# Optimization experiments

Hardware: AMD Instinct MI355X
Metric: run time of the kernel (lower is better)

## Reference

```python
import jax, jax.numpy as jnp
import numpy as np

DIM = 768
N_HEADS = 12
HEAD_DIM = DIM // N_HEADS  # 64
SEQ = 4096
ROPE_THETA = 10000.0  # local layer (layer_id=1)
WINDOW = 128          # local_attention; mask is distance <= WINDOW // 2


def setup_inputs() -> dict:
    key = jax.random.key(0)
    k1, k2, k3 = jax.random.split(key, 3)
    x = jax.random.normal(k1, (1, SEQ, DIM), dtype=jnp.float32)
    position_ids = jnp.arange(SEQ, dtype=jnp.int64 if jax.config.jax_enable_x64 else jnp.int32).reshape(1, SEQ)
    wqkv = jax.random.normal(k2, (3 * DIM, DIM), dtype=jnp.float32) * 0.02
    wo = jax.random.normal(k3, (DIM, DIM), dtype=jnp.float32) * 0.02
    return {"x": x, "position_ids": position_ids, "wqkv": wqkv, "wo": wo}


def _rope_cos_sin(position_ids):
    # inv_freq over even dims, freqs duplicated to full head_dim
    inv_freq = 1.0 / (ROPE_THETA ** (jnp.arange(0, HEAD_DIM, 2, dtype=jnp.float32) / HEAD_DIM))
    pos = position_ids.reshape(-1).astype(jnp.float32)           # [S]
    freqs = pos[:, None] * inv_freq[None, :]                      # [S, hd/2]
    freqs = jnp.concatenate([freqs, freqs], axis=-1)              # [S, hd]
    return jnp.cos(freqs)[None, None], jnp.sin(freqs)[None, None]  # [1,1,S,hd]


def _rotate_half(t):
    h = t.shape[-1] // 2
    return jnp.concatenate([-t[..., h:], t[..., :h]], axis=-1)


def reference(x, position_ids, wqkv, wo):
    bsz, seq_len, _ = x.shape
    qkv = jnp.einsum("bsd,ed->bse", x, wqkv)                      # [B,S,3*dim]
    qkv = qkv.reshape(bsz, seq_len, 3, N_HEADS, HEAD_DIM)
    qkv = jnp.transpose(qkv, (0, 3, 2, 1, 4))                      # [B,H,3,S,hd]
    q, k, v = qkv[:, :, 0], qkv[:, :, 1], qkv[:, :, 2]             # [B,H,S,hd]

    cos, sin = _rope_cos_sin(position_ids)
    q = q * cos + _rotate_half(q) * sin
    k = k * cos + _rotate_half(k) * sin

    scale = HEAD_DIM ** -0.5
    scores = jnp.einsum("bhqd,bhkd->bhqk", q, k) * scale           # [B,H,S,S]

    # sliding-window mask: |i - j| <= WINDOW // 2
    idx = jnp.arange(seq_len)
    dist = jnp.abs(idx[None, :] - idx[:, None])                    # [S,S]
    window_mask = dist <= (WINDOW // 2)
    scores = jnp.where(window_mask[None, None], scores, -jnp.inf)

    attn = jax.nn.softmax(scores, axis=-1)
    out = jnp.einsum("bhqk,bhkd->bhqd", attn, v)                   # [B,H,S,hd]
    out = jnp.transpose(out, (0, 2, 1, 3)).reshape(bsz, seq_len, DIM)
    out = jnp.einsum("bsd,ed->bse", out, wo)
    return out
```

## Files before the change

kernel.cpp:

```cpp
#include <hip/hip_runtime.h>
#include <math.h>

#define SEQ 4096
#define DIM 768
#define NH 12
#define HD 64
#define QKV_N 2304
#define HALF_WIN 64

typedef __attribute__((ext_vector_type(8))) short bf16x8;
typedef __attribute__((ext_vector_type(4))) float floatx4;

__device__ __forceinline__ unsigned short f2bf(float f) {
    unsigned u = __float_as_uint(f);
    unsigned r = (u + 0x7fffu + ((u >> 16) & 1u)) >> 16;
    return (unsigned short)r;
}

__device__ __forceinline__ void gld16(const void* g, void* l) {
    __builtin_amdgcn_global_load_lds(
        (const __attribute__((address_space(1))) unsigned*)g,
        (__attribute__((address_space(3))) unsigned*)l, 16, 0, 0);
}

__device__ __forceinline__ void fast_sc(float x, float* s, float* c) {
    float r = x * 0.15915494309189535f;
    r = r - floorf(r);
    *s = __builtin_amdgcn_sinf(r);
    *c = __builtin_amdgcn_cosf(r);
}

__global__ __launch_bounds__(256) void cast3_bf16(const float* __restrict__ x,
                                                  const float* __restrict__ wqkv,
                                                  const float* __restrict__ wo,
                                                  unsigned short* __restrict__ dst,
                                                  int nx4, int nw4, int ntot4) {
    int i = blockIdx.x * 256 + threadIdx.x;
    if (i >= ntot4) return;
    const float4* src;
    int off;
    if (i < nx4)            { src = (const float4*)x;    off = i; }
    else if (i < nx4 + nw4) { src = (const float4*)wqkv; off = i - nx4; }
    else                    { src = (const float4*)wo;   off = i - nx4 - nw4; }
    float4 v = src[off];
    ushort4 r;
    r.x = f2bf(v.x); r.y = f2bf(v.y); r.z = f2bf(v.z); r.w = f2bf(v.w);
    *(ushort4*)(dst + (size_t)i * 4) = r;
}

__global__ __launch_bounds__(256) void gemm_qkv_rope(const unsigned short* __restrict__ A,
                                                     const unsigned short* __restrict__ B,
                                                     unsigned short* __restrict__ qr,
                                                     unsigned short* __restrict__ kr,
                                                     unsigned short* __restrict__ vt) {
    __shared__ __align__(16) short smem[8192];
    short* As = smem;
    short* Bs = smem + 4096;
    const int t  = threadIdx.x;
    const int wv = t >> 6, ln = t & 63;
    const int bm0 = blockIdx.y * 64;
    const int bn0 = blockIdx.x * 64;
    const int lrow = ln >> 3;
    const int lu   = ln & 7;
    const int frow = ln & 15;
    const int q    = ln >> 4;
    const int K = DIM;

    const unsigned short* gptr[4];
    short* lptr[4];
#pragma unroll
    for (int i = 0; i < 4; i++) {
        int idx = wv * 4 + i;
        int c   = (idx < 8) ? idx : idx - 8;
        int row = c * 8 + lrow;
        int g   = (lu ^ (row & 7)) << 3;
        if (idx < 8) {
            gptr[i] = A + (size_t)(bm0 + row) * K + g;
            lptr[i] = As + c * 512;
        } else {
            gptr[i] = B + (size_t)(bn0 + row) * K + g;
            lptr[i] = Bs + c * 512;
        }
    }

    floatx4 acc[4];
#pragma unroll
    for (int j = 0; j < 4; j++) acc[j] = (floatx4){0.f, 0.f, 0.f, 0.f};

    for (int k0 = 0; k0 < K; k0 += 64) {
        __syncthreads();
#pragma unroll
        for (int i = 0; i < 4; i++) gld16(gptr[i] + k0, (void*)lptr[i]);
        __syncthreads();

#pragma unroll
        for (int ks = 0; ks < 2; ks++) {
            bf16x8 af, bfr[4];
            {
                int ra = wv * 16 + frow;
                af = *(const bf16x8*)&As[ra * 64 + (((ks * 4 + q) ^ (ra & 7)) << 3)];
            }
#pragma unroll
            for (int nt = 0; nt < 4; nt++) {
                int rb = nt * 16 + frow;
                bfr[nt] = *(const bf16x8*)&Bs[rb * 64 + (((ks * 4 + q) ^ (rb & 7)) << 3)];
            }
#pragma unroll
            for (int nt = 0; nt < 4; nt++)
                acc[nt] = __builtin_amdgcn_mfma_f32_16x16x32_bf16(
                    af, bfr[nt], acc[nt], 0, 0, 0);
        }
    }

    const int cn = frow;
    const int part = (bn0 >= 1536) ? 2 : (bn0 >= 768 ? 1 : 0);

    if (part < 2) {
        const int colw = bn0 - part * 768;
        const int h = colw >> 6;
        unsigned short* dst = (part == 0 ? qr : kr) + (size_t)h * SEQ * HD;
        const float invf0 = exp2f(-(float)cn * 0.4152410118609203f);
        const float invf1 = exp2f(-(float)(cn + 16) * 0.4152410118609203f);
        const int sbase = bm0 + wv * 16 + q * 4;
#pragma unroll
        for (int r = 0; r < 4; r++) {
            float ss = (float)(sbase + r);
            float sn0, cs0, sn1, cs1;
            fast_sc(ss * invf0, &sn0, &cs0);
            fast_sc(ss * invf1, &sn1, &cs1);
            float o0 = acc[0][r] * cs0 - acc[2][r] * sn0;
            float o1 = acc[1][r] * cs1 - acc[3][r] * sn1;
            float o2 = acc[2][r] * cs0 + acc[0][r] * sn0;
            float o3 = acc[3][r] * cs1 + acc[1][r] * sn1;
            unsigned short* p = dst + (size_t)(sbase + r) * HD + cn;
            p[0]  = f2bf(o0);
            p[16] = f2bf(o1);
            p[32] = f2bf(o2);
            p[48] = f2bf(o3);
        }
    } else {
        short* vstage = smem;
        __syncthreads();
#pragma unroll
        for (int nt = 0; nt < 4; nt++) {
            int d    = nt * 16 + cn;
            int sloc = wv * 16 + q * 4;
            ushort4 pk;
            pk.x = f2bf(acc[nt][0]);
            pk.y = f2bf(acc[nt][1]);
            pk.z = f2bf(acc[nt][2]);
            pk.w = f2bf(acc[nt][3]);
            *(ushort4*)&vstage[d * 72 + sloc] = pk;
        }
        __syncthreads();
        const int dr = t >> 2, sh = (t & 3) * 16;
        const int vcol = bn0 - 1536 + dr;
        unsigned short* vp = vt + (size_t)vcol * SEQ + bm0 + sh;
        *(uint4*)(vp)     = *(const uint4*)&vstage[dr * 72 + sh];
        *(uint4*)(vp + 8) = *(const uint4*)&vstage[dr * 72 + sh + 8];
    }
}

__global__ __launch_bounds__(256) void gemm_out(const unsigned short* __restrict__ A,
                                                const unsigned short* __restrict__ B,
                                                float* __restrict__ C,
                                                int M, int N, int K) {
    __shared__ __align__(16) short As[64 * 64];
    __shared__ __align__(16) short Bs[64 * 64];
    const int t  = threadIdx.x;
    const int wv = t >> 6, ln = t & 63;
    const int wm = wv >> 1, wn = wv & 1;
    const int bm0 = blockIdx.y * 64;
    const int bn0 = blockIdx.x * 64;
    const int lrow = ln >> 3;
    const int lu   = ln & 7;
    const int frow = ln & 15;
    const int q    = ln >> 4;

    const unsigned short* gptr[4];
    short* lptr[4];
#pragma unroll
    for (int i = 0; i < 4; i++) {
        int idx = wv * 4 + i;
        int c   = (idx < 8) ? idx : idx - 8;
        int row = c * 8 + lrow;
        int g   = (lu ^ (row & 7)) << 3;
        if (idx < 8) {
            gptr[i] = A + (size_t)(bm0 + row) * K + g;
            lptr[i] = As + c * 512;
        } else {
            gptr[i] = B + (size_t)(bn0 + row) * K + g;
            lptr[i] = Bs + c * 512;
        }
    }

    floatx4 acc[2][2];
#pragma unroll
    for (int i = 0; i < 2; i++)
#pragma unroll
        for (int j = 0; j < 2; j++) acc[i][j] = (floatx4){0.f, 0.f, 0.f, 0.f};

    for (int k0 = 0; k0 < K; k0 += 64) {
        __syncthreads();
#pragma unroll
        for (int i = 0; i < 4; i++) gld16(gptr[i] + k0, (void*)lptr[i]);
        __syncthreads();

#pragma unroll
        for (int ks = 0; ks < 2; ks++) {
            bf16x8 af[2], bfr[2];
#pragma unroll
            for (int mt = 0; mt < 2; mt++) {
                int ra = wm * 32 + mt * 16 + frow;
                af[mt] = *(const bf16x8*)&As[ra * 64 + (((ks * 4 + q) ^ (ra & 7)) << 3)];
            }
#pragma unroll
            for (int nt = 0; nt < 2; nt++) {
                int rb = wn * 32 + nt * 16 + frow;
                bfr[nt] = *(const bf16x8*)&Bs[rb * 64 + (((ks * 4 + q) ^ (rb & 7)) << 3)];
            }
#pragma unroll
            for (int mt = 0; mt < 2; mt++)
#pragma unroll
                for (int nt = 0; nt < 2; nt++)
                    acc[mt][nt] = __builtin_amdgcn_mfma_f32_16x16x32_bf16(
                        af[mt], bfr[nt], acc[mt][nt], 0, 0, 0);
        }
    }

    const int cn = ln & 15;
    const int rb4 = (ln >> 4) * 4;
#pragma unroll
    for (int mt = 0; mt < 2; mt++) {
#pragma unroll
        for (int nt = 0; nt < 2; nt++) {
            floatx4 v = acc[mt][nt];
            float* cp = C + (size_t)(bm0 + wm * 32 + mt * 16 + rb4) * N +
                        bn0 + wn * 32 + nt * 16 + cn;
#pragma unroll
            for (int r = 0; r < 4; r++) cp[(size_t)r * N] = v[r];
        }
    }
}

__global__ __launch_bounds__(512) void attn_mfma(const unsigned short* __restrict__ Q,
                                                 const unsigned short* __restrict__ K,
                                                 const unsigned short* __restrict__ Vt,
                                                 unsigned short* __restrict__ Out) {
    __shared__ __align__(16) short lds[16384];
    short* Ks  = lds;
    short* Vts = lds + 4096;
    short* Pb  = lds + 8192;
    const int t  = threadIdx.x;
    const int wv = t >> 6, ln = t & 63;
    const int h  = blockIdx.x, qs = blockIdx.y * 128;
    const int frow = ln & 15, qd = ln >> 4;
    const int rl = ln >> 3, uu = ln & 7;
    const unsigned short* Qh = Q + (size_t)h * SEQ * HD;
    const unsigned short* Kh = K + (size_t)h * SEQ * HD;
    const unsigned short* Vh = Vt + (size_t)h * HD * SEQ;

    const unsigned short* qp = Qh + (size_t)(qs + wv * 16 + frow) * HD;
    bf16x8 af0 = *(const bf16x8*)(qp + qd * 8);
    bf16x8 af1 = *(const bf16x8*)(qp + (qd + 4) * 8);

    floatx4 accO[4];
#pragma unroll
    for (int i = 0; i < 4; i++) accO[i] = (floatx4){0.f, 0.f, 0.f, 0.f};
    float m_r[4] = {-1e30f, -1e30f, -1e30f, -1e30f};
    float l_r[4] = {0.f, 0.f, 0.f, 0.f};

    const int qlo = wv * 16;

    for (int c = 0; c < 4; c++) {
        const int kb  = qs - 64 + c * 64;
        const int kbc = kb < 0 ? 0 : (kb > SEQ - 64 ? SEQ - 64 : kb);
        __syncthreads();
        {
            int row = wv * 8 + rl;
            int g = uu ^ ((row + (row >> 3)) & 7);
            gld16(Kh + (size_t)(kbc + row) * HD + g * 8, (void*)(Ks + wv * 512));
            gld16(Vh + (size_t)row * SEQ + kbc + g * 8, (void*)(Vts + wv * 512));
        }
        __syncthreads();

        const int klo0 = c * 64 - 64;
        bool live_kt[4];
        bool any_live = false;
#pragma unroll
        for (int kt = 0; kt < 4; kt++) {
            int d0 = qlo - (klo0 + kt * 16);
            live_kt[kt] = (d0 <= 64) && (d0 >= -64);
            any_live = any_live || live_kt[kt];
        }

        float sv[4][4];
        float cm[4] = {-1e30f, -1e30f, -1e30f, -1e30f};
        if (any_live) {
#pragma unroll
            for (int kt = 0; kt < 4; kt++) {
                if (live_kt[kt]) {
                    int brow = kt * 16 + frow;
                    int bz = (brow + (brow >> 3)) & 7;
                    bf16x8 b0 = *(const bf16x8*)&Ks[brow * 64 + ((qd ^ bz) << 3)];
                    bf16x8 b1 = *(const bf16x8*)&Ks[brow * 64 + (((qd + 4) ^ bz) << 3)];
                    floatx4 z = (floatx4){0.f, 0.f, 0.f, 0.f};
                    z = __builtin_amdgcn_mfma_f32_16x16x32_bf16(af0, b0, z, 0, 0, 0);
                    z = __builtin_amdgcn_mfma_f32_16x16x32_bf16(af1, b1, z, 0, 0, 0);
                    int gk = kb + kt * 16 + frow;
#pragma unroll
                    for (int r = 0; r < 4; r++) {
                        int gq = qs + wv * 16 + qd * 4 + r;
                        int dd = gq - gk;
                        bool valid = (gk >= 0) && (gk < SEQ) &&
                                     (dd <= HALF_WIN) && (dd >= -HALF_WIN);
                        float x = valid ? z[r] * 0.125f : -1e30f;
                        sv[kt][r] = x;
                        cm[r] = fmaxf(cm[r], x);
                    }
                } else {
#pragma unroll
                    for (int r = 0; r < 4; r++) sv[kt][r] = -1e30f;
                }
            }
#pragma unroll
            for (int off = 1; off < 16; off <<= 1)
#pragma unroll
                for (int r = 0; r < 4; r++)
                    cm[r] = fmaxf(cm[r], __shfl_xor(cm[r], off, 64));
            float al[4], ls[4];
#pragma unroll
            for (int r = 0; r < 4; r++) {
                float mn = fmaxf(m_r[r], cm[r]);
                al[r] = __expf(m_r[r] - mn);
                m_r[r] = mn;
                ls[r] = 0.f;
            }
            const int qrb = wv * 16 + qd * 4;
#pragma unroll
            for (int kt = 0; kt < 4; kt++) {
                int klocal = kt * 16 + frow;
                int ku = klocal >> 3;
                if (live_kt[kt]) {
#pragma unroll
                    for (int r = 0; r < 4; r++) {
                        float p = (sv[kt][r] > -1e29f) ? __expf(sv[kt][r] - m_r[r]) : 0.f;
                        ls[r] += p;
                        int qrow = qrb + r;
                        int pz = (qrow + (qrow >> 3)) & 7;
                        Pb[qrow * 64 + ((ku ^ pz) << 3) + (klocal & 7)] = (short)f2bf(p);
                    }
                } else {
#pragma unroll
                    for (int r = 0; r < 4; r++) {
                        int qrow = qrb + r;
                        int pz = (qrow + (qrow >> 3)) & 7;
                        Pb[qrow * 64 + ((ku ^ pz) << 3) + (klocal & 7)] = 0;
                    }
                }
            }
#pragma unroll
            for (int off = 1; off < 16; off <<= 1)
#pragma unroll
                for (int r = 0; r < 4; r++) ls[r] += __shfl_xor(ls[r], off, 64);
#pragma unroll
            for (int r = 0; r < 4; r++) l_r[r] = l_r[r] * al[r] + ls[r];
#pragma unroll
            for (int dt = 0; dt < 4; dt++)
#pragma unroll
                for (int r = 0; r < 4; r++) accO[dt][r] *= al[r];
        }
        __syncthreads();

        if (any_live) {
            const int prow = wv * 16 + frow;
            const int pz2 = (prow + (prow >> 3)) & 7;
            bf16x8 pa0 = *(const bf16x8*)&Pb[prow * 64 + ((qd ^ pz2) << 3)];
            bf16x8 pa1 = *(const bf16x8*)&Pb[prow * 64 + (((qd + 4) ^ pz2) << 3)];
#pragma unroll
            for (int dt = 0; dt < 4; dt++) {
                int vrow = dt * 16 + frow;
                int vz = (vrow + (vrow >> 3)) & 7;
                bf16x8 v0 = *(const bf16x8*)&Vts[vrow * 64 + ((qd ^ vz) << 3)];
                bf16x8 v1 = *(const bf16x8*)&Vts[vrow * 64 + (((qd + 4) ^ vz) << 3)];
                accO[dt] = __builtin_amdgcn_mfma_f32_16x16x32_bf16(pa0, v0, accO[dt], 0, 0, 0);
                accO[dt] = __builtin_amdgcn_mfma_f32_16x16x32_bf16(pa1, v1, accO[dt], 0, 0, 0);
            }
        }
    }

    __syncthreads();
    short* Ob = lds;
    float linv[4];
#pragma unroll
    for (int r = 0; r < 4; r++) linv[r] = 1.0f / l_r[r];
#pragma unroll
    for (int dt = 0; dt < 4; dt++)
#pragma unroll
        for (int r = 0; r < 4; r++) {
            int qrow = wv * 16 + qd * 4 + r;
            int dcol = dt * 16 + frow;
            Ob[qrow * 72 + dcol] = (short)f2bf(accO[dt][r] * linv[r]);
        }
    __syncthreads();
    const int orow = t >> 2, og = (t & 3) * 16;
    uint4 a = *(const uint4*)&Ob[orow * 72 + og];
    uint4 b = *(const uint4*)&Ob[orow * 72 + og + 8];
    unsigned short* op = Out + (size_t)(qs + orow) * DIM + h * HD + og;
    *(uint4*)(op)     = a;
    *(uint4*)(op + 8) = b;
}

extern "C" void kernel_launch(void* const* d_in, const int* in_sizes, int n_in,
                              void* d_out, int out_size, void* d_ws, size_t ws_size,
                              hipStream_t stream) {
    const float* x    = (const float*)d_in[0];
    const float* wqkv = (const float*)d_in[2];
    const float* wo   = (const float*)d_in[3];
    float* out = (float*)d_out;

    unsigned short* q_r  = (unsigned short*)d_ws;
    unsigned short* k_r  = q_r + (size_t)NH * SEQ * HD;
    unsigned short* v_t  = k_r + (size_t)NH * SEQ * HD;
    unsigned short* x_bf = v_t + (size_t)NH * SEQ * HD;
    unsigned short* wqkv_bf = x_bf + (size_t)SEQ * DIM;
    unsigned short* wo_bf   = wqkv_bf + (size_t)QKV_N * DIM;
    unsigned short* attn_bf = wo_bf + (size_t)DIM * DIM;

    const int nx4 = SEQ * DIM / 4;
    const int nw4 = QKV_N * DIM / 4;
    const int no4 = DIM * DIM / 4;
    const int ntot4 = nx4 + nw4 + no4;

    cast3_bf16<<<dim3((ntot4 + 255) / 256), 256, 0, stream>>>(
        x, wqkv, wo, x_bf, nx4, nw4, ntot4);
    gemm_qkv_rope<<<dim3(QKV_N / 64, SEQ / 64), 256, 0, stream>>>(
        x_bf, wqkv_bf, q_r, k_r, v_t);
    attn_mfma<<<dim3(NH, SEQ / 128), 512, 0, stream>>>(
        q_r, k_r, v_t, attn_bf);
    gemm_out<<<dim3(DIM / 64, SEQ / 64), 256, 0, stream>>>(
        attn_bf, wo_bf, out, SEQ, DIM, DIM);
}
```

Before: 129.0 us.

## Double-buffer LDS tiles in QKV and output GEMMs to overlap loads

Both GEMM kernels now use two LDS buffers and prefetch the next K-slice with global_load_lds while computing on the current one, cutting one of the two barriers per iteration. The aim is to hide global-to-LDS latency behind MFMA work. It doubles LDS use to 32KB per block, which may lower occupancy. It also relies on the single barrier at the end of each iteration covering both completion of the async LDS loads and safe reuse of the buffer.

```diff
diff --git a/kernel.cpp b/kernel.cpp
--- a/kernel.cpp
+++ b/kernel.cpp
@@ -53,9 +53,7 @@
                                                      unsigned short* __restrict__ qr,
                                                      unsigned short* __restrict__ kr,
                                                      unsigned short* __restrict__ vt) {
-    __shared__ __align__(16) short smem[8192];
-    short* As = smem;
-    short* Bs = smem + 4096;
+    __shared__ __align__(16) short smem[16384];
     const int t  = threadIdx.x;
     const int wv = t >> 6, ln = t & 63;
     const int bm0 = blockIdx.y * 64;
@@ -67,7 +65,7 @@
     const int K = DIM;
 
     const unsigned short* gptr[4];
-    short* lptr[4];
+    int loff[4];
 #pragma unroll
     for (int i = 0; i < 4; i++) {
         int idx = wv * 4 + i;
@@ -76,10 +74,10 @@
         int g   = (lu ^ (row & 7)) << 3;
         if (idx < 8) {
             gptr[i] = A + (size_t)(bm0 + row) * K + g;
-            lptr[i] = As + c * 512;
+            loff[i] = c * 512;
         } else {
             gptr[i] = B + (size_t)(bn0 + row) * K + g;
-            lptr[i] = Bs + c * 512;
+            loff[i] = 4096 + c * 512;
         }
     }
 
@@ -87,12 +85,21 @@
 #pragma unroll
     for (int j = 0; j < 4; j++) acc[j] = (floatx4){0.f, 0.f, 0.f, 0.f};
 
-    for (int k0 = 0; k0 < K; k0 += 64) {
-        __syncthreads();
-#pragma unroll
-        for (int i = 0; i < 4; i++) gld16(gptr[i] + k0, (void*)lptr[i]);
-        __syncthreads();
-
+#pragma unroll
+    for (int i = 0; i < 4; i++) gld16(gptr[i], (void*)(smem + loff[i]));
+    __syncthreads();
+
+    int cur = 0;
+    for (int it = 0; it < 12; it++) {
+        if (it + 1 < 12) {
+            int nb = cur ^ 1;
+            int k0n = (it + 1) * 64;
+#pragma unroll
+            for (int i = 0; i < 4; i++)
+                gld16(gptr[i] + k0n, (void*)(smem + nb * 8192 + loff[i]));
+        }
+        short* As = smem + cur * 8192;
+        short* Bs = As + 4096;
 #pragma unroll
         for (int ks = 0; ks < 2; ks++) {
             bf16x8 af, bfr[4];
@@ -110,6 +117,8 @@
                 acc[nt] = __builtin_amdgcn_mfma_f32_16x16x32_bf16(
                     af, bfr[nt], acc[nt], 0, 0, 0);
         }
+        __syncthreads();
+        cur ^= 1;
     }
 
     const int cn = frow;
@@ -140,7 +149,6 @@
         }
     } else {
         short* vstage = smem;
-        __syncthreads();
 #pragma unroll
         for (int nt = 0; nt < 4; nt++) {
             int d    = nt * 16 + cn;
@@ -165,8 +173,7 @@
                                                 const unsigned short* __restrict__ B,
                                                 float* __restrict__ C,
                                                 int M, int N, int K) {
-    __shared__ __align__(16) short As[64 * 64];
-    __shared__ __align__(16) short Bs[64 * 64];
+    __shared__ __align__(16) short smem[16384];
     const int t  = threadIdx.x;
     const int wv = t >> 6, ln = t & 63;
     const int wm = wv >> 1, wn = wv & 1;
@@ -178,7 +185,7 @@
     const int q    = ln >> 4;
 
     const unsigned short* gptr[4];
-    short* lptr[4];
+    int loff[4];
 #pragma unroll
     for (int i = 0; i < 4; i++) {
         int idx = wv * 4 + i;
@@ -187,10 +194,10 @@
         int g   = (lu ^ (row & 7)) << 3;
         if (idx < 8) {
             gptr[i] = A + (size_t)(bm0 + row) * K + g;
-            lptr[i] = As + c * 512;
+            loff[i] = c * 512;
         } else {
             gptr[i] = B + (size_t)(bn0 + row) * K + g;
-            lptr[i] = Bs + c * 512;
+            loff[i] = 4096 + c * 512;
         }
     }
 
@@ -200,12 +207,22 @@
 #pragma unroll
         for (int j = 0; j < 2; j++) acc[i][j] = (floatx4){0.f, 0.f, 0.f, 0.f};
 
-    for (int k0 = 0; k0 < K; k0 += 64) {
-        __syncthreads();
-#pragma unroll
-        for (int i = 0; i < 4; i++) gld16(gptr[i] + k0, (void*)lptr[i]);
-        __syncthreads();
-
+#pragma unroll
+    for (int i = 0; i < 4; i++) gld16(gptr[i], (void*)(smem + loff[i]));
+    __syncthreads();
+
+    int cur = 0;
+    const int NIT = K / 64;
+    for (int it = 0; it < NIT; it++) {
+        if (it + 1 < NIT) {
+            int nb = cur ^ 1;
+            int k0n = (it + 1) * 64;
+#pragma unroll
+            for (int i = 0; i < 4; i++)
+                gld16(gptr[i] + k0n, (void*)(smem + nb * 8192 + loff[i]));
+        }
+        short* As = smem + cur * 8192;
+        short* Bs = As + 4096;
 #pragma unroll
         for (int ks = 0; ks < 2; ks++) {
             bf16x8 af[2], bfr[2];
@@ -226,6 +243,8 @@
                     acc[mt][nt] = __builtin_amdgcn_mfma_f32_16x16x32_bf16(
                         af[mt], bfr[nt], acc[mt][nt], 0, 0, 0);
         }
+        __syncthreads();
+        cur ^= 1;
     }
 
     const int cn = ln & 15;
```

Measured after the change: 128.8 us. No clear change (-0.1%).
